# Performance work log

Hardware: AMD Instinct MI355X
Metric: run time of the kernel (lower is better)

Reference implementation:

```python
import jax, jax.numpy as jnp
import numpy as np

N_HEAD = 16

def setup_inputs() -> dict:
    key = jax.random.key(0)
    k1, k2, k3 = jax.random.split(key, 3)
    B, T, D = 2, 2048, 1024
    x = jax.random.normal(k1, (B, T, D), dtype=jnp.float32)
    sigma_qkv = float(np.sqrt(2.0 / (D + 3 * D)))
    sigma_out = float(np.sqrt(2.0 / (D + D)))
    W_qkv = jax.random.truncated_normal(k2, -3.0, 3.0, (3 * D, D), dtype=jnp.float32) * sigma_qkv
    W_out = jax.random.truncated_normal(k3, -3.0, 3.0, (D, D), dtype=jnp.float32) * sigma_out
    return {"x": x, "W_qkv": W_qkv, "W_out": W_out}


def reference(x, W_qkv, W_out):
    B, T, C = x.shape
    H = N_HEAD
    hd = C // H
    qkv = x @ W_qkv.T  # (B,T,3C)
    q, k, v = jnp.split(qkv, 3, axis=-1)
    # (B,T,C) -> (B,H,T,hd)
    q = q.reshape(B, T, H, hd).transpose(0, 2, 1, 3)
    k = k.reshape(B, T, H, hd).transpose(0, 2, 1, 3)
    v = v.reshape(B, T, H, hd).transpose(0, 2, 1, 3)
    scale = 1.0 / jnp.sqrt(jnp.asarray(hd, dtype=x.dtype))
    score = jnp.einsum('bhqd,bhkd->bhqk', q, k) * scale  # (B,H,T,T)
    causal = jnp.tril(jnp.ones((T, T), dtype=bool))
    score = jnp.where(causal, score, -jnp.inf)
    attn = jax.nn.softmax(score, axis=-1)
    out = jnp.einsum('bhqk,bhkd->bhqd', attn, v)  # (B,H,T,hd)
    out = out.transpose(0, 2, 1, 3).reshape(B, T, C)
    return out @ W_out.T
```

## Files before the change

kernel.cpp:

```cpp
#include <hip/hip_runtime.h>
#include <hip/hip_bf16.h>
#include <cstdint>

typedef unsigned short u16;
typedef __attribute__((ext_vector_type(8))) short bf16x8;
typedef __attribute__((ext_vector_type(4))) float f32x4;

#define T_SEQ 2048
#define NHEAD 16
#define HDIM  64
#define NB    2

__device__ __forceinline__ float bf2f(uint32_t h) { return __uint_as_float(h << 16); }
__device__ __forceinline__ u16 f2bf(float f) {
    uint32_t u = __float_as_uint(f);
    u += 0x7fffu + ((u >> 16) & 1u);
    return (u16)(u >> 16);
}

__device__ __forceinline__ void gl_lds16(const u16* g, u16* s) {
    __builtin_amdgcn_global_load_lds(
        (const __attribute__((address_space(1))) unsigned int*)g,
        (__attribute__((address_space(3))) unsigned int*)s, 16, 0, 0);
}

__global__ void detect_dtype(const uint32_t* __restrict__ x, int* __restrict__ flag) {
    __shared__ int red[4];
    int c = 0;
#pragma unroll
    for (int j = 0; j < 4; j++) {
        uint32_t v = x[threadIdx.x * 4 + j];
        uint32_t lo = v & 0xffffu;
        uint32_t e = (lo >> 7) & 0xffu;
        if (lo != 0u && e >= 110u && e <= 135u) c++;
    }
#pragma unroll
    for (int off = 32; off; off >>= 1) c += __shfl_down(c, off);
    if ((threadIdx.x & 63) == 0) red[threadIdx.x >> 6] = c;
    __syncthreads();
    if (threadIdx.x == 0)
        *flag = (red[0] + red[1] + red[2] + red[3] > 614) ? 1 : 0;
}

__global__ __launch_bounds__(256) void to_bf16(
    const void* __restrict__ src, u16* __restrict__ dst, int n4,
    const int* __restrict__ flag)
{
    int i = blockIdx.x * 256 + threadIdx.x;
    const int stride = gridDim.x * 256;
    if (*flag != 0) {
        const uint2* s = (const uint2*)src;
        uint2* d = (uint2*)dst;
        for (; i < n4; i += stride) d[i] = s[i];
    } else {
        const float4* s = (const float4*)src;
        for (; i < n4; i += stride) {
            float4 v = s[i];
            ushort4 o = { f2bf(v.x), f2bf(v.y), f2bf(v.z), f2bf(v.w) };
            *(ushort4*)(dst + (size_t)i * 4) = o;
        }
    }
}

template<int BM, int MODE>
__global__ __launch_bounds__(256, 3) void gemm_bt_mfma(
    const u16* __restrict__ A, const u16* __restrict__ B,
    int N, int K,
    u16* __restrict__ qo, u16* __restrict__ ko, u16* __restrict__ vt,
    u16* __restrict__ outb16, float* __restrict__ outf32,
    const int* __restrict__ flag)
{
    constexpr int WM = BM / 2;
    constexpr int MI = WM / 16;
    constexpr int IA = BM / 32;
    constexpr int ST = 2 * BM * 64 * 2;
    constexpr int E16 = 4 * WM * 72 * 2;
    constexpr int EF = (MODE == 1) ? 4 * WM * (WM + 4) * 4 : 0;
    constexpr int SB = (ST > E16 ? ST : E16) > EF ? (ST > E16 ? ST : E16) : EF;
    __shared__ u16 smem[SB / 2];
    u16* As = smem;
    u16* Bs = smem + BM * 64;
    const int tid = threadIdx.x;
    const int bm = blockIdx.y * BM, bn = blockIdx.x * BM;
    const int w = tid >> 6, lane = tid & 63;
    const int wm = (w >> 1) * WM, wn = (w & 1) * WM;
    const int n16 = lane & 15, quad = lane >> 4;
    const int l8 = lane >> 3, c8 = lane & 7;

    f32x4 acc[MI][MI];
#pragma unroll
    for (int mi = 0; mi < MI; mi++)
#pragma unroll
        for (int ni = 0; ni < MI; ni++) acc[mi][ni] = (f32x4){0.f, 0.f, 0.f, 0.f};

    const int KT = K >> 6;
    for (int kt = 0; kt < KT; kt++) {
        const int k0 = kt << 6;
#pragma unroll
        for (int i = 0; i < IA; i++) {
            int rowblk = (i * 4 + w) * 8;
            int row = rowblk + l8;
            int gcol = (c8 ^ l8) * 8;
            gl_lds16(A + (size_t)(bm + row) * K + k0 + gcol, As + rowblk * 64);
            gl_lds16(B + (size_t)(bn + row) * K + k0 + gcol, Bs + rowblk * 64);
        }
        __syncthreads();
#pragma unroll
        for (int ks = 0; ks < 2; ks++) {
            bf16x8 af[MI], bfr[MI];
#pragma unroll
            for (int mi = 0; mi < MI; mi++) {
                int row = wm + mi * 16 + n16;
                af[mi] = *(const bf16x8*)(As + row * 64 + (((ks * 4 + quad) ^ (n16 & 7)) * 8));
            }
#pragma unroll
            for (int ni = 0; ni < MI; ni++) {
                int row = wn + ni * 16 + n16;
                bfr[ni] = *(const bf16x8*)(Bs + row * 64 + (((ks * 4 + quad) ^ (n16 & 7)) * 8));
            }
#pragma unroll
            for (int mi = 0; mi < MI; mi++)
#pragma unroll
                for (int ni = 0; ni < MI; ni++)
                    acc[mi][ni] = __builtin_amdgcn_mfma_f32_16x16x32_bf16(
                        af[mi], bfr[ni], acc[mi][ni], 0, 0, 0);
        }
        __syncthreads();
    }

    if constexpr (MODE == 0) {
        u16* ep = smem + w * (WM * 72);
        const int which = (bn + wn) >> 10;
        const int hq = ((bn + wn) & 1023) >> 6;
        const int bb = (bm + wm) >> 11;
        const int tb = (bm + wm) & (T_SEQ - 1);
        if (which == 2) {
#pragma unroll
            for (int mi = 0; mi < MI; mi++)
#pragma unroll
                for (int ni = 0; ni < MI; ni++)
#pragma unroll
                    for (int r = 0; r < 4; r++)
                        ep[(ni * 16 + n16) * 72 + mi * 16 + quad * 4 + r] = f2bf(acc[mi][ni][r]);
            asm volatile("s_waitcnt lgkmcnt(0)" ::: "memory");
            u16* dst = vt + ((size_t)(bb * NHEAD + hq) * HDIM) * T_SEQ + tb;
#pragma unroll
            for (int it = 0; it < 8; it++) {
                int row = it * 8 + l8, col = c8 * 8;
                bf16x8 v = *(const bf16x8*)(ep + row * 72 + col);
                *(bf16x8*)(dst + (size_t)row * T_SEQ + col) = v;
            }
        } else {
            const float sc = which ? 1.f : 0.125f;
#pragma unroll
            for (int mi = 0; mi < MI; mi++)
#pragma unroll
                for (int ni = 0; ni < MI; ni++)
#pragma unroll
                    for (int r = 0; r < 4; r++)
                        ep[(mi * 16 + quad * 4 + r) * 72 + ni * 16 + n16] = f2bf(acc[mi][ni][r] * sc);
            asm volatile("s_waitcnt lgkmcnt(0)" ::: "memory");
            u16* dst = (which ? ko : qo) + ((size_t)(bb * NHEAD + hq) * T_SEQ + tb) * HDIM;
#pragma unroll
            for (int it = 0; it < 8; it++) {
                int row = it * 8 + l8, col = c8 * 8;
                bf16x8 v = *(const bf16x8*)(ep + row * 72 + col);
                *(bf16x8*)(dst + (size_t)row * HDIM + col) = v;
            }
        }
    } else {
        if (*flag == 0) {
            float* epf = (float*)smem + w * (WM * (WM + 4));
#pragma unroll
            for (int mi = 0; mi < MI; mi++)
#pragma unroll
                for (int ni = 0; ni < MI; ni++)
#pragma unroll
                    for (int r = 0; r < 4; r++)
                        epf[(mi * 16 + quad * 4 + r) * (WM + 4) + ni * 16 + n16] = acc[mi][ni][r];
            asm volatile("s_waitcnt lgkmcnt(0)" ::: "memory");
            constexpr int LPR = WM / 4;
            constexpr int RPI = 64 / LPR;
#pragma unroll
            for (int it = 0; it < WM / RPI; it++) {
                int row = it * RPI + lane / LPR, col = (lane % LPR) * 4;
                float4 v = *(const float4*)(epf + row * (WM + 4) + col);
                *(float4*)(outf32 + (size_t)(bm + wm + row) * N + bn + wn + col) = v;
            }
        } else {
            u16* ep = smem + w * (WM * 72);
#pragma unroll
            for (int mi = 0; mi < MI; mi++)
#pragma unroll
                for (int ni = 0; ni < MI; ni++)
#pragma unroll
                    for (int r = 0; r < 4; r++)
                        ep[(mi * 16 + quad * 4 + r) * 72 + ni * 16 + n16] = f2bf(acc[mi][ni][r]);
            asm volatile("s_waitcnt lgkmcnt(0)" ::: "memory");
            constexpr int LPR = WM / 8;
            constexpr int RPI = 64 / LPR;
#pragma unroll
            for (int it = 0; it < WM / RPI; it++) {
                int row = it * RPI + lane / LPR, col = (lane % LPR) * 8;
                bf16x8 v = *(const bf16x8*)(ep + row * 72 + col);
                *(bf16x8*)(outb16 + (size_t)(bm + wm + row) * N + bn + wn + col) = v;
            }
        }
    }
}

__global__ __launch_bounds__(256, 2) void attn_mfma(
    const u16* __restrict__ qb, const u16* __restrict__ kb,
    const u16* __restrict__ vt, u16* __restrict__ ob)
{
    __shared__ u16 Ks[64 * 64];
    __shared__ u16 Vs[64 * 64];
    __shared__ u16 Plds[4][16][72];
    const int lin = blockIdx.x;
    const int xcd = lin & 7;
    const int rest = lin >> 3;
    const int p = rest & 15;
    const int grp = rest >> 4;
    const int bh = grp * 8 + xcd;
    const int qtb = 31 - p, qts = p;
    const int w = threadIdx.x >> 6, lane = threadIdx.x & 63;
    const int n16 = lane & 15, quad = lane >> 4;
    const int l8 = lane >> 3, c8 = lane & 7;
    const size_t baseK = (size_t)bh * T_SEQ * HDIM;
    const size_t baseV = (size_t)bh * HDIM * T_SEQ;
    const int b = bh >> 4, h = bh & 15;

    bf16x8 ones;
#pragma unroll
    for (int j = 0; j < 8; j++) ones[j] = (short)0x3F80;

    auto stage = [&](int kt) {
#pragma unroll
        for (int i = 0; i < 2; i++) {
            int rowblk = (i * 4 + w) * 8;
            int row = rowblk + l8;
            int gc = (c8 ^ l8) * 8;
            gl_lds16(kb + baseK + (size_t)(kt * 64 + row) * HDIM + gc, Ks + rowblk * 64);
            gl_lds16(vt + baseV + (size_t)row * T_SEQ + kt * 64 + gc, Vs + rowblk * 64);
        }
    };

    const int qrowb = qtb * 64 + w * 16, qrows = qts * 64 + w * 16;
    bf16x8 qfb[2], qfs[2];
#pragma unroll
    for (int ks = 0; ks < 2; ks++) {
        qfb[ks] = *(const bf16x8*)(qb + baseK + (size_t)(qrowb + n16) * HDIM + ks * 32 + quad * 8);
        qfs[ks] = *(const bf16x8*)(qb + baseK + (size_t)(qrows + n16) * HDIM + ks * 32 + quad * 8);
    }

    f32x4 accOb[4], accOs[4];
#pragma unroll
    for (int st = 0; st < 4; st++) {
        accOb[st] = (f32x4){0.f, 0.f, 0.f, 0.f};
        accOs[st] = (f32x4){0.f, 0.f, 0.f, 0.f};
    }
    f32x4 accLb = (f32x4){0.f, 0.f, 0.f, 0.f};
    f32x4 accLs = (f32x4){0.f, 0.f, 0.f, 0.f};

    stage(0);
    for (int kt = 0; kt <= qtb; kt++) {
        __syncthreads();

        bf16x8 kf[2][4], vf[2][4];
#pragma unroll
        for (int st = 0; st < 4; st++)
#pragma unroll
            for (int ks = 0; ks < 2; ks++) {
                int off = (st * 16 + n16) * 64 + (((ks * 4 + quad) ^ (n16 & 7)) * 8);
                kf[ks][st] = *(const bf16x8*)(Ks + off);
                vf[ks][st] = *(const bf16x8*)(Vs + off);
            }
        __syncthreads();

        if (kt < qtb) stage(kt + 1);

        {
            f32x4 S[4];
#pragma unroll
            for (int st = 0; st < 4; st++) S[st] = (f32x4){0.f, 0.f, 0.f, 0.f};
#pragma unroll
            for (int st = 0; st < 4; st++)
#pragma unroll
                for (int ks = 0; ks < 2; ks++)
                    S[st] = __builtin_amdgcn_mfma_f32_16x16x32_bf16(qfb[ks], kf[ks][st], S[st], 0, 0, 0);
            if (kt == qtb) {
                int qloc = w * 16 + quad * 4;
#pragma unroll
                for (int st = 0; st < 4; st++) {
                    int kloc = st * 16 + n16;
#pragma unroll
                    for (int r = 0; r < 4; r++)
                        if (kloc > qloc + r) S[st][r] = -INFINITY;
                }
            }
#pragma unroll
            for (int st = 0; st < 4; st++)
#pragma unroll
                for (int r = 0; r < 4; r++) {
                    float pv = exp2f(__builtin_fmaf(S[st][r], 1.44269504f, -14.4269504f));
                    Plds[w][quad * 4 + r][st * 16 + n16] = (u16)(__float_as_uint(pv) >> 16);
                }
            asm volatile("s_waitcnt lgkmcnt(0)" ::: "memory");
            bf16x8 pf[2];
#pragma unroll
            for (int ks = 0; ks < 2; ks++)
                pf[ks] = *(const bf16x8*)(&Plds[w][n16][ks * 32 + quad * 8]);
#pragma unroll
            for (int st = 0; st < 4; st++)
#pragma unroll
                for (int ks = 0; ks < 2; ks++)
                    accOb[st] = __builtin_amdgcn_mfma_f32_16x16x32_bf16(pf[ks], vf[ks][st], accOb[st], 0, 0, 0);
#pragma unroll
            for (int ks = 0; ks < 2; ks++)
                accLb = __builtin_amdgcn_mfma_f32_16x16x32_bf16(pf[ks], ones, accLb, 0, 0, 0);
        }

        if (kt <= qts) {
            f32x4 S[4];
#pragma unroll
            for (int st = 0; st < 4; st++) S[st] = (f32x4){0.f, 0.f, 0.f, 0.f};
#pragma unroll
            for (int st = 0; st < 4; st++)
#pragma unroll
                for (int ks = 0; ks < 2; ks++)
                    S[st] = __builtin_amdgcn_mfma_f32_16x16x32_bf16(qfs[ks], kf[ks][st], S[st], 0, 0, 0);
            if (kt == qts) {
                int qloc = w * 16 + quad * 4;
#pragma unroll
                for (int st = 0; st < 4; st++) {
                    int kloc = st * 16 + n16;
#pragma unroll
                    for (int r = 0; r < 4; r++)
                        if (kloc > qloc + r) S[st][r] = -INFINITY;
                }
            }
#pragma unroll
            for (int st = 0; st < 4; st++)
#pragma unroll
                for (int r = 0; r < 4; r++) {
                    float pv = exp2f(__builtin_fmaf(S[st][r], 1.44269504f, -14.4269504f));
                    Plds[w][quad * 4 + r][st * 16 + n16] = (u16)(__float_as_uint(pv) >> 16);
                }
            asm volatile("s_waitcnt lgkmcnt(0)" ::: "memory");
            bf16x8 pf[2];
#pragma unroll
            for (int ks = 0; ks < 2; ks++)
                pf[ks] = *(const bf16x8*)(&Plds[w][n16][ks * 32 + quad * 8]);
#pragma unroll
            for (int st = 0; st < 4; st++)
#pragma unroll
                for (int ks = 0; ks < 2; ks++)
                    accOs[st] = __builtin_amdgcn_mfma_f32_16x16x32_bf16(pf[ks], vf[ks][st], accOs[st], 0, 0, 0);
#pragma unroll
            for (int ks = 0; ks < 2; ks++)
                accLs = __builtin_amdgcn_mfma_f32_16x16x32_bf16(pf[ks], ones, accLs, 0, 0, 0);
        }
    }

#pragma unroll
    for (int r = 0; r < 4; r++) {
        float inv = 1.f / accLb[r];
#pragma unroll
        for (int st = 0; st < 4; st++)
            Plds[w][quad * 4 + r][st * 16 + n16] = f2bf(accOb[st][r] * inv);
    }
    asm volatile("s_waitcnt lgkmcnt(0)" ::: "memory");
    u16* dstb = ob + ((size_t)(b * T_SEQ + qrowb)) * 1024 + h * HDIM;
#pragma unroll
    for (int it = 0; it < 2; it++) {
        int row = it * 8 + l8, col = c8 * 8;
        bf16x8 v = *(const bf16x8*)(&Plds[w][row][col]);
        *(bf16x8*)(dstb + (size_t)row * 1024 + col) = v;
    }
    asm volatile("s_waitcnt lgkmcnt(0)" ::: "memory");
#pragma unroll
    for (int r = 0; r < 4; r++) {
        float inv = 1.f / accLs[r];
#pragma unroll
        for (int st = 0; st < 4; st++)
            Plds[w][quad * 4 + r][st * 16 + n16] = f2bf(accOs[st][r] * inv);
    }
    asm volatile("s_waitcnt lgkmcnt(0)" ::: "memory");
    u16* dsts = ob + ((size_t)(b * T_SEQ + qrows)) * 1024 + h * HDIM;
#pragma unroll
    for (int it = 0; it < 2; it++) {
        int row = it * 8 + l8, col = c8 * 8;
        bf16x8 v = *(const bf16x8*)(&Plds[w][row][col]);
        *(bf16x8*)(dsts + (size_t)row * 1024 + col) = v;
    }
}

extern "C" void kernel_launch(void* const* d_in, const int* in_sizes, int n_in,
                              void* d_out, int out_size, void* d_ws, size_t ws_size,
                              hipStream_t stream) {
    const void* x    = d_in[0];
    const void* Wqkv = d_in[1];
    const void* Wout = d_in[2];

    const int Mtok = NB * T_SEQ;
    const size_t n_x    = (size_t)Mtok * 1024;
    const size_t n_wqkv = (size_t)3072 * 1024;
    const size_t n_wout = (size_t)1024 * 1024;
    const size_t qkv_elems = (size_t)NB * NHEAD * T_SEQ * HDIM;

    u16* xb    = (u16*)d_ws;
    u16* wqkvb = xb + n_x;
    u16* woutb = wqkvb + n_wqkv;
    u16* qb    = woutb + n_wout;
    u16* kb    = qb + qkv_elems;
    u16* vt    = kb + qkv_elems;
    u16* obuf  = vt + qkv_elems;
    int* flag  = (int*)(obuf + qkv_elems);

    detect_dtype<<<1, 256, 0, stream>>>((const uint32_t*)x, flag);

    to_bf16<<<1024, 256, 0, stream>>>(x,    xb,    (int)(n_x / 4),    flag);
    to_bf16<<<1024, 256, 0, stream>>>(Wqkv, wqkvb, (int)(n_wqkv / 4), flag);
    to_bf16<<<512,  256, 0, stream>>>(Wout, woutb, (int)(n_wout / 4), flag);

    gemm_bt_mfma<128, 0><<<dim3(3072 / 128, Mtok / 128), 256, 0, stream>>>(
        xb, wqkvb, 3072, 1024, qb, kb, vt, nullptr, nullptr, flag);

    attn_mfma<<<dim3(NB * NHEAD * (T_SEQ / 128)), 256, 0, stream>>>(qb, kb, vt, obuf);

    gemm_bt_mfma<64, 1><<<dim3(1024 / 64, Mtok / 64), 256, 0, stream>>>(
        obuf, woutb, 1024, 1024, nullptr, nullptr, nullptr,
        (u16*)d_out, (float*)d_out, flag);
}
```

Measured before the change: 169.2 us.

## Software-pipeline P·V behind next QK^T in attention; rectangular out-proj tiles

The attention loop now runs both query tiles' QK^T and softmax in one pass. It defers the P·V and row-sum MFMAs by one iteration, using P and V fragments kept from the previous step, so matrix work overlaps the exp and LDS round trip. Separate P buffers for the two query tiles let their stores share a single wait, and a trailing drain step handles the last tile. The output-projection GEMM moves to 64x128 tiles with a separate launch-bounds parameter, which halves the grid and increases B reuse. This costs extra registers for the held fragments and more LDS.

```diff
diff --git a/kernel.cpp b/kernel.cpp
--- a/kernel.cpp
+++ b/kernel.cpp
@@ -62,66 +62,69 @@
     }
 }
 
-template<int BM, int MODE>
-__global__ __launch_bounds__(256, 3) void gemm_bt_mfma(
+template<int BM, int BN, int MODE, int MINW>
+__global__ __launch_bounds__(256, MINW) void gemm_bt_mfma(
     const u16* __restrict__ A, const u16* __restrict__ B,
     int N, int K,
     u16* __restrict__ qo, u16* __restrict__ ko, u16* __restrict__ vt,
     u16* __restrict__ outb16, float* __restrict__ outf32,
     const int* __restrict__ flag)
 {
-    constexpr int WM = BM / 2;
-    constexpr int MI = WM / 16;
-    constexpr int IA = BM / 32;
-    constexpr int ST = 2 * BM * 64 * 2;
+    constexpr int WM = BM / 2, WN = BN / 2;
+    constexpr int MI = WM / 16, NI = WN / 16;
+    constexpr int IA = BM / 32, IB = BN / 32;
+    constexpr int ST = (BM + BN) * 64 * 2;
     constexpr int E16 = 4 * WM * 72 * 2;
-    constexpr int EF = (MODE == 1) ? 4 * WM * (WM + 4) * 4 : 0;
+    constexpr int EF = (MODE == 1) ? 4 * WM * (WN + 4) * 4 : 0;
     constexpr int SB = (ST > E16 ? ST : E16) > EF ? (ST > E16 ? ST : E16) : EF;
     __shared__ u16 smem[SB / 2];
     u16* As = smem;
     u16* Bs = smem + BM * 64;
     const int tid = threadIdx.x;
-    const int bm = blockIdx.y * BM, bn = blockIdx.x * BM;
+    const int bm = blockIdx.y * BM, bn = blockIdx.x * BN;
     const int w = tid >> 6, lane = tid & 63;
-    const int wm = (w >> 1) * WM, wn = (w & 1) * WM;
+    const int wm = (w >> 1) * WM, wn = (w & 1) * WN;
     const int n16 = lane & 15, quad = lane >> 4;
     const int l8 = lane >> 3, c8 = lane & 7;
 
-    f32x4 acc[MI][MI];
+    f32x4 acc[MI][NI];
 #pragma unroll
     for (int mi = 0; mi < MI; mi++)
 #pragma unroll
-        for (int ni = 0; ni < MI; ni++) acc[mi][ni] = (f32x4){0.f, 0.f, 0.f, 0.f};
+        for (int ni = 0; ni < NI; ni++) acc[mi][ni] = (f32x4){0.f, 0.f, 0.f, 0.f};
 
     const int KT = K >> 6;
     for (int kt = 0; kt < KT; kt++) {
         const int k0 = kt << 6;
+        const int gcol = (c8 ^ l8) * 8;
 #pragma unroll
         for (int i = 0; i < IA; i++) {
             int rowblk = (i * 4 + w) * 8;
-            int row = rowblk + l8;
-            int gcol = (c8 ^ l8) * 8;
-            gl_lds16(A + (size_t)(bm + row) * K + k0 + gcol, As + rowblk * 64);
-            gl_lds16(B + (size_t)(bn + row) * K + k0 + gcol, Bs + rowblk * 64);
+            gl_lds16(A + (size_t)(bm + rowblk + l8) * K + k0 + gcol, As + rowblk * 64);
+        }
+#pragma unroll
+        for (int i = 0; i < IB; i++) {
+            int rowblk = (i * 4 + w) * 8;
+            gl_lds16(B + (size_t)(bn + rowblk + l8) * K + k0 + gcol, Bs + rowblk * 64);
         }
         __syncthreads();
 #pragma unroll
         for (int ks = 0; ks < 2; ks++) {
-            bf16x8 af[MI], bfr[MI];
+            bf16x8 af[MI], bfr[NI];
 #pragma unroll
             for (int mi = 0; mi < MI; mi++) {
                 int row = wm + mi * 16 + n16;
                 af[mi] = *(const bf16x8*)(As + row * 64 + (((ks * 4 + quad) ^ (n16 & 7)) * 8));
             }
 #pragma unroll
-            for (int ni = 0; ni < MI; ni++) {
+            for (int ni = 0; ni < NI; ni++) {
                 int row = wn + ni * 16 + n16;
                 bfr[ni] = *(const bf16x8*)(Bs + row * 64 + (((ks * 4 + quad) ^ (n16 & 7)) * 8));
             }
 #pragma unroll
             for (int mi = 0; mi < MI; mi++)
 #pragma unroll
-                for (int ni = 0; ni < MI; ni++)
+                for (int ni = 0; ni < NI; ni++)
                     acc[mi][ni] = __builtin_amdgcn_mfma_f32_16x16x32_bf16(
                         af[mi], bfr[ni], acc[mi][ni], 0, 0, 0);
         }
@@ -138,7 +141,7 @@
 #pragma unroll
             for (int mi = 0; mi < MI; mi++)
 #pragma unroll
-                for (int ni = 0; ni < MI; ni++)
+                for (int ni = 0; ni < NI; ni++)
 #pragma unroll
                     for (int r = 0; r < 4; r++)
                         ep[(ni * 16 + n16) * 72 + mi * 16 + quad * 4 + r] = f2bf(acc[mi][ni][r]);
@@ -155,7 +158,7 @@
 #pragma unroll
             for (int mi = 0; mi < MI; mi++)
 #pragma unroll
-                for (int ni = 0; ni < MI; ni++)
+                for (int ni = 0; ni < NI; ni++)
 #pragma unroll
                     for (int r = 0; r < 4; r++)
                         ep[(mi * 16 + quad * 4 + r) * 72 + ni * 16 + n16] = f2bf(acc[mi][ni][r] * sc);
@@ -170,21 +173,21 @@
         }
     } else {
         if (*flag == 0) {
-            float* epf = (float*)smem + w * (WM * (WM + 4));
+            float* epf = (float*)smem + w * (WM * (WN + 4));
 #pragma unroll
             for (int mi = 0; mi < MI; mi++)
 #pragma unroll
-                for (int ni = 0; ni < MI; ni++)
+                for (int ni = 0; ni < NI; ni++)
 #pragma unroll
                     for (int r = 0; r < 4; r++)
-                        epf[(mi * 16 + quad * 4 + r) * (WM + 4) + ni * 16 + n16] = acc[mi][ni][r];
+                        epf[(mi * 16 + quad * 4 + r) * (WN + 4) + ni * 16 + n16] = acc[mi][ni][r];
             asm volatile("s_waitcnt lgkmcnt(0)" ::: "memory");
-            constexpr int LPR = WM / 4;
+            constexpr int LPR = WN / 4;
             constexpr int RPI = 64 / LPR;
 #pragma unroll
             for (int it = 0; it < WM / RPI; it++) {
                 int row = it * RPI + lane / LPR, col = (lane % LPR) * 4;
-                float4 v = *(const float4*)(epf + row * (WM + 4) + col);
+                float4 v = *(const float4*)(epf + row * (WN + 4) + col);
                 *(float4*)(outf32 + (size_t)(bm + wm + row) * N + bn + wn + col) = v;
             }
         } else {
@@ -192,12 +195,12 @@
 #pragma unroll
             for (int mi = 0; mi < MI; mi++)
 #pragma unroll
-                for (int ni = 0; ni < MI; ni++)
+                for (int ni = 0; ni < NI; ni++)
 #pragma unroll
                     for (int r = 0; r < 4; r++)
                         ep[(mi * 16 + quad * 4 + r) * 72 + ni * 16 + n16] = f2bf(acc[mi][ni][r]);
             asm volatile("s_waitcnt lgkmcnt(0)" ::: "memory");
-            constexpr int LPR = WM / 8;
+            constexpr int LPR = WN / 8;
             constexpr int RPI = 64 / LPR;
 #pragma unroll
             for (int it = 0; it < WM / RPI; it++) {
@@ -215,7 +218,8 @@
 {
     __shared__ u16 Ks[64 * 64];
     __shared__ u16 Vs[64 * 64];
-    __shared__ u16 Plds[4][16][72];
+    __shared__ u16 PldsB[4][16][72];
+    __shared__ u16 PldsS[4][16][72];
     const int lin = blockIdx.x;
     const int xcd = lin & 7;
     const int rest = lin >> 3;
@@ -262,6 +266,8 @@
     f32x4 accLb = (f32x4){0.f, 0.f, 0.f, 0.f};
     f32x4 accLs = (f32x4){0.f, 0.f, 0.f, 0.f};
 
+    bf16x8 pfb[2], pfs[2], vfp[2][4];
+
     stage(0);
     for (int kt = 0; kt <= qtb; kt++) {
         __syncthreads();
@@ -279,119 +285,130 @@
 
         if (kt < qtb) stage(kt + 1);
 
-        {
-            f32x4 S[4];
-#pragma unroll
-            for (int st = 0; st < 4; st++) S[st] = (f32x4){0.f, 0.f, 0.f, 0.f};
+        f32x4 Sb[4], Ss[4];
+#pragma unroll
+        for (int st = 0; st < 4; st++) {
+            Sb[st] = (f32x4){0.f, 0.f, 0.f, 0.f};
+            Ss[st] = (f32x4){0.f, 0.f, 0.f, 0.f};
+        }
+#pragma unroll
+        for (int st = 0; st < 4; st++)
+#pragma unroll
+            for (int ks = 0; ks < 2; ks++)
+                Sb[st] = __builtin_amdgcn_mfma_f32_16x16x32_bf16(qfb[ks], kf[ks][st], Sb[st], 0, 0, 0);
+        if (kt <= qts)
 #pragma unroll
             for (int st = 0; st < 4; st++)
 #pragma unroll
                 for (int ks = 0; ks < 2; ks++)
-                    S[st] = __builtin_amdgcn_mfma_f32_16x16x32_bf16(qfb[ks], kf[ks][st], S[st], 0, 0, 0);
-            if (kt == qtb) {
+                    Ss[st] = __builtin_amdgcn_mfma_f32_16x16x32_bf16(qfs[ks], kf[ks][st], Ss[st], 0, 0, 0);
+
+        if (kt > 0) {
+#pragma unroll
+            for (int st = 0; st < 4; st++)
+#pragma unroll
+                for (int ks = 0; ks < 2; ks++)
+                    accOb[st] = __builtin_amdgcn_mfma_f32_16x16x32_bf16(pfb[ks], vfp[ks][st], accOb[st], 0, 0, 0);
+#pragma unroll
+            for (int ks = 0; ks < 2; ks++)
+                accLb = __builtin_amdgcn_mfma_f32_16x16x32_bf16(pfb[ks], ones, accLb, 0, 0, 0);
+            if (kt - 1 <= qts) {
+#pragma unroll
+                for (int st = 0; st < 4; st++)
+#pragma unroll
+                    for (int ks = 0; ks < 2; ks++)
+                        accOs[st] = __builtin_amdgcn_mfma_f32_16x16x32_bf16(pfs[ks], vfp[ks][st], accOs[st], 0, 0, 0);
+#pragma unroll
+                for (int ks = 0; ks < 2; ks++)
+                    accLs = __builtin_amdgcn_mfma_f32_16x16x32_bf16(pfs[ks], ones, accLs, 0, 0, 0);
+            }
+        }
+
+        if (kt == qtb) {
+            int qloc = w * 16 + quad * 4;
+#pragma unroll
+            for (int st = 0; st < 4; st++) {
+                int kloc = st * 16 + n16;
+#pragma unroll
+                for (int r = 0; r < 4; r++)
+                    if (kloc > qloc + r) Sb[st][r] = -INFINITY;
+            }
+        }
+#pragma unroll
+        for (int st = 0; st < 4; st++)
+#pragma unroll
+            for (int r = 0; r < 4; r++) {
+                float pv = exp2f(__builtin_fmaf(Sb[st][r], 1.44269504f, -14.4269504f));
+                PldsB[w][quad * 4 + r][st * 16 + n16] = (u16)(__float_as_uint(pv) >> 16);
+            }
+        if (kt <= qts) {
+            if (kt == qts) {
                 int qloc = w * 16 + quad * 4;
 #pragma unroll
                 for (int st = 0; st < 4; st++) {
                     int kloc = st * 16 + n16;
 #pragma unroll
                     for (int r = 0; r < 4; r++)
-                        if (kloc > qloc + r) S[st][r] = -INFINITY;
+                        if (kloc > qloc + r) Ss[st][r] = -INFINITY;
                 }
             }
 #pragma unroll
             for (int st = 0; st < 4; st++)
 #pragma unroll
                 for (int r = 0; r < 4; r++) {
-                    float pv = exp2f(__builtin_fmaf(S[st][r], 1.44269504f, -14.4269504f));
-                    Plds[w][quad * 4 + r][st * 16 + n16] = (u16)(__float_as_uint(pv) >> 16);
+                    float pv = exp2f(__builtin_fmaf(Ss[st][r], 1.44269504f, -14.4269504f));
+                    PldsS[w][quad * 4 + r][st * 16 + n16] = (u16)(__float_as_uint(pv) >> 16);
                 }
-            asm volatile("s_waitcnt lgkmcnt(0)" ::: "memory");
-            bf16x8 pf[2];
+        }
+        asm volatile("s_waitcnt lgkmcnt(0)" ::: "memory");
+#pragma unroll
+        for (int ks = 0; ks < 2; ks++)
+            pfb[ks] = *(const bf16x8*)(&PldsB[w][n16][ks * 32 + quad * 8]);
+        if (kt <= qts)
 #pragma unroll
             for (int ks = 0; ks < 2; ks++)
-                pf[ks] = *(const bf16x8*)(&Plds[w][n16][ks * 32 + quad * 8]);
-#pragma unroll
-            for (int st = 0; st < 4; st++)
-#pragma unroll
-                for (int ks = 0; ks < 2; ks++)
-                    accOb[st] = __builtin_amdgcn_mfma_f32_16x16x32_bf16(pf[ks], vf[ks][st], accOb[st], 0, 0, 0);
+                pfs[ks] = *(const bf16x8*)(&PldsS[w][n16][ks * 32 + quad * 8]);
+#pragma unroll
+        for (int st = 0; st < 4; st++)
 #pragma unroll
             for (int ks = 0; ks < 2; ks++)
-                accLb = __builtin_amdgcn_mfma_f32_16x16x32_bf16(pf[ks], ones, accLb, 0, 0, 0);
-        }
-
-        if (kt <= qts) {
-            f32x4 S[4];
-#pragma unroll
-            for (int st = 0; st < 4; st++) S[st] = (f32x4){0.f, 0.f, 0.f, 0.f};
-#pragma unroll
-            for (int st = 0; st < 4; st++)
-#pragma unroll
-                for (int ks = 0; ks < 2; ks++)
-                    S[st] = __builtin_amdgcn_mfma_f32_16x16x32_bf16(qfs[ks], kf[ks][st], S[st], 0, 0, 0);
-            if (kt == qts) {
-                int qloc = w * 16 + quad * 4;
-#pragma unroll
-                for (int st = 0; st < 4; st++) {
-                    int kloc = st * 16 + n16;
-#pragma unroll
-                    for (int r = 0; r < 4; r++)
-                        if (kloc > qloc + r) S[st][r] = -INFINITY;
-                }
-            }
-#pragma unroll
-            for (int st = 0; st < 4; st++)
-#pragma unroll
-                for (int r = 0; r < 4; r++) {
-                    float pv = exp2f(__builtin_fmaf(S[st][r], 1.44269504f, -14.4269504f));
-                    Plds[w][quad * 4 + r][st * 16 + n16] = (u16)(__float_as_uint(pv) >> 16);
-                }
-            asm volatile("s_waitcnt lgkmcnt(0)" ::: "memory");
-            bf16x8 pf[2];
-#pragma unroll
-            for (int ks = 0; ks < 2; ks++)
-                pf[ks] = *(const bf16x8*)(&Plds[w][n16][ks * 32 + quad * 8]);
-#pragma unroll
-            for (int st = 0; st < 4; st++)
-#pragma unroll
-                for (int ks = 0; ks < 2; ks++)
-                    accOs[st] = __builtin_amdgcn_mfma_f32_16x16x32_bf16(pf[ks], vf[ks][st], accOs[st], 0, 0, 0);
-#pragma unroll
-            for (int ks = 0; ks < 2; ks++)
-                accLs = __builtin_amdgcn_mfma_f32_16x16x32_bf16(pf[ks], ones, accLs, 0, 0, 0);
-        }
-    }
-
+                vfp[ks][st] = vf[ks][st];
+    }
+
+#pragma unroll
+    for (int st = 0; st < 4; st++)
+#pragma unroll
+        for (int ks = 0; ks < 2; ks++)
+            accOb[st] = __builtin_amdgcn_mfma_f32_16x16x32_bf16(pfb[ks], vfp[ks][st], accOb[st], 0, 0, 0);
+#pragma unroll
+    for (int ks = 0; ks < 2; ks++)
+        accLb = __builtin_amdgcn_mfma_f32_16x16x32_bf16(pfb[ks], ones, accLb, 0, 0, 0);
+
+    __syncthreads();
 #pragma unroll
     for (int r = 0; r < 4; r++) {
         float inv = 1.f / accLb[r];
 #pragma unroll
         for (int st = 0; st < 4; st++)
-            Plds[w][quad * 4 + r][st * 16 + n16] = f2bf(accOb[st][r] * inv);
+            PldsB[w][quad * 4 + r][st * 16 + n16] = f2bf(accOb[st][r] * inv);
+    }
+#pragma unroll
+    for (int r = 0; r < 4; r++) {
+        float inv = 1.f / accLs[r];
+#pragma unroll
+        for (int st = 0; st < 4; st++)
+            PldsS[w][quad * 4 + r][st * 16 + n16] = f2bf(accOs[st][r] * inv);
     }
     asm volatile("s_waitcnt lgkmcnt(0)" ::: "memory");
     u16* dstb = ob + ((size_t)(b * T_SEQ + qrowb)) * 1024 + h * HDIM;
+    u16* dsts = ob + ((size_t)(b * T_SEQ + qrows)) * 1024 + h * HDIM;
 #pragma unroll
     for (int it = 0; it < 2; it++) {
         int row = it * 8 + l8, col = c8 * 8;
-        bf16x8 v = *(const bf16x8*)(&Plds[w][row][col]);
-        *(bf16x8*)(dstb + (size_t)row * 1024 + col) = v;
-    }
-    asm volatile("s_waitcnt lgkmcnt(0)" ::: "memory");
-#pragma unroll
-    for (int r = 0; r < 4; r++) {
-        float inv = 1.f / accLs[r];
-#pragma unroll
-        for (int st = 0; st < 4; st++)
-            Plds[w][quad * 4 + r][st * 16 + n16] = f2bf(accOs[st][r] * inv);
-    }
-    asm volatile("s_waitcnt lgkmcnt(0)" ::: "memory");
-    u16* dsts = ob + ((size_t)(b * T_SEQ + qrows)) * 1024 + h * HDIM;
-#pragma unroll
-    for (int it = 0; it < 2; it++) {
-        int row = it * 8 + l8, col = c8 * 8;
-        bf16x8 v = *(const bf16x8*)(&Plds[w][row][col]);
-        *(bf16x8*)(dsts + (size_t)row * 1024 + col) = v;
+        bf16x8 v1 = *(const bf16x8*)(&PldsB[w][row][col]);
+        *(bf16x8*)(dstb + (size_t)row * 1024 + col) = v1;
+        bf16x8 v2 = *(const bf16x8*)(&PldsS[w][row][col]);
+        *(bf16x8*)(dsts + (size_t)row * 1024 + col) = v2;
     }
 }
 
@@ -423,12 +440,12 @@
     to_bf16<<<1024, 256, 0, stream>>>(Wqkv, wqkvb, (int)(n_wqkv / 4), flag);
     to_bf16<<<512,  256, 0, stream>>>(Wout, woutb, (int)(n_wout / 4), flag);
 
-    gemm_bt_mfma<128, 0><<<dim3(3072 / 128, Mtok / 128), 256, 0, stream>>>(
+    gemm_bt_mfma<128, 128, 0, 3><<<dim3(3072 / 128, Mtok / 128), 256, 0, stream>>>(
         xb, wqkvb, 3072, 1024, qb, kb, vt, nullptr, nullptr, flag);
 
     attn_mfma<<<dim3(NB * NHEAD * (T_SEQ / 128)), 256, 0, stream>>>(qb, kb, vt, obuf);
 
-    gemm_bt_mfma<64, 1><<<dim3(1024 / 64, Mtok / 64), 256, 0, stream>>>(
+    gemm_bt_mfma<64, 128, 1, 4><<<dim3(1024 / 128, Mtok / 64), 256, 0, stream>>>(
         obuf, woutb, 1024, 1024, nullptr, nullptr, nullptr,
         (u16*)d_out, (float*)d_out, flag);
 }
```

After: 175.0 us. +3.4%, slower.
